# Performance work log

Hardware: AMD Instinct MI355X
Metric: run time of the kernel (lower is better)

The kernel has to match this reference:

```python
import jax, jax.numpy as jnp
import numpy as np

H = 64  # rnn_size == input_size

def setup_inputs() -> dict:
    key = jax.random.key(0)
    ks = jax.random.split(key, 6)
    vocab = 32000
    B, T = 4096, 128
    s = 1.0 / np.sqrt(H)
    return {
        "inst": jax.random.randint(ks[0], (B, T), 0, vocab, dtype=jnp.int64),
        "embed_w": jax.random.normal(ks[1], (vocab + 1, H), dtype=jnp.float32),
        "W_ih": jax.random.uniform(ks[2], (4 * H, H), dtype=jnp.float32, minval=-s, maxval=s),
        "W_hh": jax.random.uniform(ks[3], (4 * H, H), dtype=jnp.float32, minval=-s, maxval=s),
        "b_ih": jax.random.uniform(ks[4], (4 * H,), dtype=jnp.float32, minval=-s, maxval=s),
        "b_hh": jax.random.uniform(ks[5], (4 * H,), dtype=jnp.float32, minval=-s, maxval=s),
    }

def _lstm_scan(xs, W_ih, W_hh, b_ih, b_hh):
    # xs: [T, B, H]. PyTorch LSTMCell gate order: i, f, g, o.
    B = xs.shape[1]
    # Precompute input projections for all timesteps in one big GEMM.
    x_proj = jnp.einsum('tbh,gh->tbg', xs, W_ih) + b_ih + b_hh  # [T, B, 4H]

    def step(carry, xp):
        h, c = carry
        gates = xp + h @ W_hh.T  # [B, 4H]
        i, f, g, o = jnp.split(gates, 4, axis=-1)
        c = jax.nn.sigmoid(f) * c + jax.nn.sigmoid(i) * jnp.tanh(g)
        h = jax.nn.sigmoid(o) * jnp.tanh(c)
        return (h, c), None

    h0 = jnp.zeros((B, H), dtype=xs.dtype)
    c0 = jnp.zeros((B, H), dtype=xs.dtype)
    (h, c), _ = jax.lax.scan(step, (h0, c0), x_proj)
    return h

def reference(inst, embed_w, W_ih, W_hh, b_ih, b_hh):
    # inst: [B, T] int; embedding lookup for whole sequence at once.
    xs = embed_w[inst]                 # [B, T, H]
    xs = jnp.swapaxes(xs, 0, 1)        # [T, B, H] for scan over time
    return _lstm_scan(xs, W_ih, W_hh, b_ih, b_hh)  # final h: [B, H]
```

## Files before the change

### kernel.cpp

```cpp
#include <hip/hip_runtime.h>
#include <hip/hip_bf16.h>

#define H_DIM   64
#define T_STEPS 128
#define B_TOT   4096
#define BB      16
#define SK      72
#define NTHREADS 512

typedef _Float16 half8  __attribute__((ext_vector_type(8)));
typedef __fp16   fp16x2 __attribute__((ext_vector_type(2)));
typedef __attribute__((ext_vector_type(4))) float f32x4;

__device__ __forceinline__ float fast_sigmoid(float x) {
    float e = __expf(-x);
    return __builtin_amdgcn_rcpf(1.0f + e);
}
__device__ __forceinline__ float fast_tanh(float x) {
    float e2 = __expf(2.0f * x);
    return 1.0f - 2.0f * __builtin_amdgcn_rcpf(e2 + 1.0f);
}

__global__ __launch_bounds__(NTHREADS) void lstm_fused(
    const int* __restrict__ inst, const float* __restrict__ embed,
    const float* __restrict__ Wih, const float* __restrict__ Whh,
    const float* __restrict__ bih, const float* __restrict__ bhh,
    float* __restrict__ out)
{
    __shared__ __align__(16) _Float16 sX[2][BB][SK];
    __shared__ __align__(16) _Float16 sH[2][BB][SK];
    __shared__ int sInst[BB * T_STEPS];

    const int tid  = (int)threadIdx.x;
    const int w    = tid >> 6;
    const int l    = tid & 63;
    const int lrow = l & 15;
    const int lk   = l >> 4;
    const bool losd = (lrow < 8);
    const int c    = w * 8 + (lrow & 7);
    const int b0   = (int)blockIdx.x * BB;

    for (int i = tid; i < BB * T_STEPS; i += NTHREADS)
        sInst[i] = inst[b0 * T_STEPS + i];

    for (int i = tid; i < BB * SK; i += NTHREADS)
        ((_Float16*)sH)[i] = (_Float16)0.0f;
    __syncthreads();

    half8 wf[2][4];
    float bias[2];
#pragma unroll
    for (int q = 0; q < 2; ++q) {
        const int gate = q * 2 + (lrow >> 3);
        const int gcol = gate * 64 + c;
        bias[q] = bih[gcol] + bhh[gcol];
#pragma unroll
        for (int kf = 0; kf < 4; ++kf) {
            const float* src = (kf < 2 ? Wih : Whh) + (long)gcol * H_DIM + (kf & 1) * 32 + lk * 8;
            half8 v;
#pragma unroll
            for (int j = 0; j < 8; ++j) v[j] = (_Float16)src[j];
            wf[q][kf] = v;
        }
    }

    const int xr = tid >> 5;
    const int xc = tid & 31;
    {
        const int idx = sInst[xr * T_STEPS + 0];
        const float2 xv = *reinterpret_cast<const float2*>(embed + (long)idx * H_DIM + xc * 2);
        fp16x2 hp = __builtin_amdgcn_cvt_pkrtz(xv.x, xv.y);
        *reinterpret_cast<fp16x2*>(&sX[0][xr][xc * 2]) = hp;
    }
    __syncthreads();

    float creg[2] = {0.f, 0.f};
    float hreg[2] = {0.f, 0.f};

    for (int t = 0; t < T_STEPS; ++t) {
        const int buf = t & 1;
        const int ob  = buf ^ 1;
        const bool pf = (t + 1 < T_STEPS);

        float2 xv = {0.f, 0.f};
        if (pf) {
            const int idx = sInst[xr * T_STEPS + t + 1];
            xv = *reinterpret_cast<const float2*>(embed + (long)idx * H_DIM + xc * 2);
        }

        half8 a0 = *reinterpret_cast<const half8*>(&sX[buf][lrow][lk * 8]);
        half8 a1 = *reinterpret_cast<const half8*>(&sX[buf][lrow][32 + lk * 8]);
        half8 a2 = *reinterpret_cast<const half8*>(&sH[buf][lrow][lk * 8]);
        half8 a3 = *reinterpret_cast<const half8*>(&sH[buf][lrow][32 + lk * 8]);

        f32x4 acc[2];
#pragma unroll
        for (int q = 0; q < 2; ++q) {
            f32x4 pA = {bias[q], bias[q], bias[q], bias[q]};
            f32x4 pB = {0.f, 0.f, 0.f, 0.f};
            pA = __builtin_amdgcn_mfma_f32_16x16x32_f16(a0, wf[q][0], pA, 0, 0, 0);
            pB = __builtin_amdgcn_mfma_f32_16x16x32_f16(a1, wf[q][1], pB, 0, 0, 0);
            pA = __builtin_amdgcn_mfma_f32_16x16x32_f16(a2, wf[q][2], pA, 0, 0, 0);
            pB = __builtin_amdgcn_mfma_f32_16x16x32_f16(a3, wf[q][3], pB, 0, 0, 0);
            acc[q] = pA + pB;
        }

        const float e0 = __shfl_xor(losd ? acc[0][2] : acc[0][0], 8);
        const float e1 = __shfl_xor(losd ? acc[0][3] : acc[0][1], 8);
        const float e2 = __shfl_xor(losd ? acc[1][2] : acc[1][0], 8);
        const float e3 = __shfl_xor(losd ? acc[1][3] : acc[1][1], 8);

#pragma unroll
        for (int j = 0; j < 2; ++j) {
            const int r  = (losd ? 0 : 2) + j;
            const float ea = j ? e1 : e0;
            const float eb = j ? e3 : e2;
            const float vi = losd ? acc[0][r] : ea;
            const float vf = losd ? ea        : acc[0][r];
            const float vg = losd ? acc[1][r] : eb;
            const float vo = losd ? eb        : acc[1][r];
            const float iv = fast_sigmoid(vi);
            const float fv = fast_sigmoid(vf);
            const float gv = fast_tanh(vg);
            const float ov = fast_sigmoid(vo);
            const float cn = fv * creg[j] + iv * gv;
            creg[j] = cn;
            hreg[j] = ov * fast_tanh(cn);

            if (pf) {
                const int row = lk * 4 + r;
                sH[ob][row][c] = (_Float16)hreg[j];
            }
        }

        if (pf) {
            fp16x2 hp = __builtin_amdgcn_cvt_pkrtz(xv.x, xv.y);
            *reinterpret_cast<fp16x2*>(&sX[ob][xr][xc * 2]) = hp;
        }
        __syncthreads();
    }

#pragma unroll
    for (int j = 0; j < 2; ++j) {
        const int row = lk * 4 + (losd ? 0 : 2) + j;
        out[(long)(b0 + row) * H_DIM + c] = hreg[j];
    }
}

extern "C" void kernel_launch(void* const* d_in, const int* in_sizes, int n_in,
                              void* d_out, int out_size, void* d_ws, size_t ws_size,
                              hipStream_t stream) {
    const int*   inst  = (const int*)  d_in[0];
    const float* embed = (const float*)d_in[1];
    const float* Wih   = (const float*)d_in[2];
    const float* Whh   = (const float*)d_in[3];
    const float* bih   = (const float*)d_in[4];
    const float* bhh   = (const float*)d_in[5];
    float* out = (float*)d_out;

    lstm_fused<<<B_TOT / BB, NTHREADS, 0, stream>>>(inst, embed, Wih, Whh, bih, bhh, out);
}
```

Baseline: 90.87 us.

## Double threads per block, one gate-tile per wave, fold log2e into weights

Doubles the block to 16 waves so each wave computes one 16x16 MFMA gate tile (4 MFMAs per step instead of 8) and each lane produces a single h/c element, using a two-stage xor shuffle to gather the i,f,g,o gates. The log2(e) and 2·log2(e) scaling is folded into the fp16 weights and bias so activations use raw exp2 instead of exp plus a multiply. The embedding prefetch becomes one scalar-broadcast row per wave with one float per lane. The aim is to shorten the serial per-step critical path, in exchange for more barrier participants per step and extra shuffle and select work; scaling the weights before the fp16 conversion slightly changes rounding.

```diff
diff --git a/kernel.cpp b/kernel.cpp
--- a/kernel.cpp
+++ b/kernel.cpp
@@ -6,19 +6,23 @@
 #define B_TOT   4096
 #define BB      16
 #define SK      72
-#define NTHREADS 512
+#define NTHREADS 1024
 
 typedef _Float16 half8  __attribute__((ext_vector_type(8)));
 typedef __fp16   fp16x2 __attribute__((ext_vector_type(2)));
 typedef __attribute__((ext_vector_type(4))) float f32x4;
 
-__device__ __forceinline__ float fast_sigmoid(float x) {
-    float e = __expf(-x);
-    return __builtin_amdgcn_rcpf(1.0f + e);
+#if __has_builtin(__builtin_amdgcn_exp2f)
+#define EXP2(x) __builtin_amdgcn_exp2f(x)
+#else
+#define EXP2(x) exp2f(x)
+#endif
+
+__device__ __forceinline__ float sigmoid2(float xp) {
+    return __builtin_amdgcn_rcpf(1.0f + EXP2(-xp));
 }
-__device__ __forceinline__ float fast_tanh(float x) {
-    float e2 = __expf(2.0f * x);
-    return 1.0f - 2.0f * __builtin_amdgcn_rcpf(e2 + 1.0f);
+__device__ __forceinline__ float tanh2(float xp) {
+    return fmaf(-2.0f, __builtin_amdgcn_rcpf(EXP2(xp) + 1.0f), 1.0f);
 }
 
 __global__ __launch_bounds__(NTHREADS) void lstm_fused(
@@ -36,9 +40,14 @@
     const int l    = tid & 63;
     const int lrow = l & 15;
     const int lk   = l >> 4;
-    const bool losd = (lrow < 8);
-    const int c    = w * 8 + (lrow & 7);
+    const int g4   = lrow >> 2;
+    const bool g0  = g4 & 1;
+    const bool g1  = (g4 >> 1) & 1;
+    const int col  = w * 4 + (lrow & 3);
+    const int row  = lk * 4 + g4;
     const int b0   = (int)blockIdx.x * BB;
+
+    const float L2E = 1.4426950408889634f;
 
     for (int i = tid; i < BB * T_STEPS; i += NTHREADS)
         sInst[i] = inst[b0 * T_STEPS + i];
@@ -47,45 +56,39 @@
         ((_Float16*)sH)[i] = (_Float16)0.0f;
     __syncthreads();
 
-    half8 wf[2][4];
-    float bias[2];
-#pragma unroll
-    for (int q = 0; q < 2; ++q) {
-        const int gate = q * 2 + (lrow >> 3);
-        const int gcol = gate * 64 + c;
-        bias[q] = bih[gcol] + bhh[gcol];
+    const float wscale = (g4 == 2) ? 2.0f * L2E : L2E;
+    half8 wf[4];
+    float bias;
+    {
+        const int gcol = g4 * 64 + col;
+        bias = (bih[gcol] + bhh[gcol]) * wscale;
 #pragma unroll
         for (int kf = 0; kf < 4; ++kf) {
             const float* src = (kf < 2 ? Wih : Whh) + (long)gcol * H_DIM + (kf & 1) * 32 + lk * 8;
             half8 v;
 #pragma unroll
-            for (int j = 0; j < 8; ++j) v[j] = (_Float16)src[j];
-            wf[q][kf] = v;
+            for (int j = 0; j < 8; ++j) v[j] = (_Float16)(src[j] * wscale);
+            wf[kf] = v;
         }
     }
 
-    const int xr = tid >> 5;
-    const int xc = tid & 31;
     {
-        const int idx = sInst[xr * T_STEPS + 0];
-        const float2 xv = *reinterpret_cast<const float2*>(embed + (long)idx * H_DIM + xc * 2);
-        fp16x2 hp = __builtin_amdgcn_cvt_pkrtz(xv.x, xv.y);
-        *reinterpret_cast<fp16x2*>(&sX[0][xr][xc * 2]) = hp;
+        const int idx = __builtin_amdgcn_readfirstlane(sInst[w * T_STEPS + 0]);
+        sX[0][w][l] = (_Float16)embed[(long)idx * H_DIM + l];
     }
     __syncthreads();
 
-    float creg[2] = {0.f, 0.f};
-    float hreg[2] = {0.f, 0.f};
+    float creg = 0.f, hreg = 0.f;
 
     for (int t = 0; t < T_STEPS; ++t) {
         const int buf = t & 1;
         const int ob  = buf ^ 1;
         const bool pf = (t + 1 < T_STEPS);
 
-        float2 xv = {0.f, 0.f};
+        float xv = 0.f;
         if (pf) {
-            const int idx = sInst[xr * T_STEPS + t + 1];
-            xv = *reinterpret_cast<const float2*>(embed + (long)idx * H_DIM + xc * 2);
+            const int idx = __builtin_amdgcn_readfirstlane(sInst[w * T_STEPS + t + 1]);
+            xv = embed[(long)idx * H_DIM + l];
         }
 
         half8 a0 = *reinterpret_cast<const half8*>(&sX[buf][lrow][lk * 8]);
@@ -93,58 +96,47 @@
         half8 a2 = *reinterpret_cast<const half8*>(&sH[buf][lrow][lk * 8]);
         half8 a3 = *reinterpret_cast<const half8*>(&sH[buf][lrow][32 + lk * 8]);
 
-        f32x4 acc[2];
-#pragma unroll
-        for (int q = 0; q < 2; ++q) {
-            f32x4 pA = {bias[q], bias[q], bias[q], bias[q]};
-            f32x4 pB = {0.f, 0.f, 0.f, 0.f};
-            pA = __builtin_amdgcn_mfma_f32_16x16x32_f16(a0, wf[q][0], pA, 0, 0, 0);
-            pB = __builtin_amdgcn_mfma_f32_16x16x32_f16(a1, wf[q][1], pB, 0, 0, 0);
-            pA = __builtin_amdgcn_mfma_f32_16x16x32_f16(a2, wf[q][2], pA, 0, 0, 0);
-            pB = __builtin_amdgcn_mfma_f32_16x16x32_f16(a3, wf[q][3], pB, 0, 0, 0);
-            acc[q] = pA + pB;
-        }
+        f32x4 pA = {bias, bias, bias, bias};
+        f32x4 pB = {0.f, 0.f, 0.f, 0.f};
+        pA = __builtin_amdgcn_mfma_f32_16x16x32_f16(a0, wf[0], pA, 0, 0, 0);
+        pB = __builtin_amdgcn_mfma_f32_16x16x32_f16(a1, wf[1], pB, 0, 0, 0);
+        pA = __builtin_amdgcn_mfma_f32_16x16x32_f16(a2, wf[2], pA, 0, 0, 0);
+        pB = __builtin_amdgcn_mfma_f32_16x16x32_f16(a3, wf[3], pB, 0, 0, 0);
+        const f32x4 acc = pA + pB;
 
-        const float e0 = __shfl_xor(losd ? acc[0][2] : acc[0][0], 8);
-        const float e1 = __shfl_xor(losd ? acc[0][3] : acc[0][1], 8);
-        const float e2 = __shfl_xor(losd ? acc[1][2] : acc[1][0], 8);
-        const float e3 = __shfl_xor(losd ? acc[1][3] : acc[1][1], 8);
+        const float s1a = g0 ? acc[0] : acc[1];
+        const float s1b = g0 ? acc[2] : acc[3];
+        const float r1a = __shfl_xor(s1a, 4);
+        const float r1b = __shfl_xor(s1b, 4);
+        const float B0 = g0 ? r1a : acc[0];
+        const float B1 = g0 ? acc[1] : r1a;
+        const float B2 = g0 ? r1b : acc[2];
+        const float B3 = g0 ? acc[3] : r1b;
+        const float s2a = g1 ? B0 : B2;
+        const float s2b = g1 ? B1 : B3;
+        const float r2a = __shfl_xor(s2a, 8);
+        const float r2b = __shfl_xor(s2b, 8);
+        const float vi = g1 ? r2a : B0;
+        const float vf = g1 ? r2b : B1;
+        const float vg = g1 ? B2 : r2a;
+        const float vo = g1 ? B3 : r2b;
 
-#pragma unroll
-        for (int j = 0; j < 2; ++j) {
-            const int r  = (losd ? 0 : 2) + j;
-            const float ea = j ? e1 : e0;
-            const float eb = j ? e3 : e2;
-            const float vi = losd ? acc[0][r] : ea;
-            const float vf = losd ? ea        : acc[0][r];
-            const float vg = losd ? acc[1][r] : eb;
-            const float vo = losd ? eb        : acc[1][r];
-            const float iv = fast_sigmoid(vi);
-            const float fv = fast_sigmoid(vf);
-            const float gv = fast_tanh(vg);
-            const float ov = fast_sigmoid(vo);
-            const float cn = fv * creg[j] + iv * gv;
-            creg[j] = cn;
-            hreg[j] = ov * fast_tanh(cn);
-
-            if (pf) {
-                const int row = lk * 4 + r;
-                sH[ob][row][c] = (_Float16)hreg[j];
-            }
-        }
+        const float iv = sigmoid2(vi);
+        const float fv = sigmoid2(vf);
+        const float gv = tanh2(vg);
+        const float ov = sigmoid2(vo);
+        const float cn = fv * creg + iv * gv;
+        creg = cn;
+        hreg = ov * tanh2(cn * (2.0f * L2E));
 
         if (pf) {
-            fp16x2 hp = __builtin_amdgcn_cvt_pkrtz(xv.x, xv.y);
-            *reinterpret_cast<fp16x2*>(&sX[ob][xr][xc * 2]) = hp;
+            sH[ob][row][col] = (_Float16)hreg;
+            sX[ob][w][l] = (_Float16)xv;
         }
         __syncthreads();
     }
 
-#pragma unroll
-    for (int j = 0; j < 2; ++j) {
-        const int row = lk * 4 + (losd ? 0 : 2) + j;
-        out[(long)(b0 + row) * H_DIM + c] = hreg[j];
-    }
+    out[(long)(b0 + row) * H_DIM + col] = hreg;
 }
 
 extern "C" void kernel_launch(void* const* d_in, const int* in_sizes, int n_in,
```

Result: slower. 104.0 us (+14.4%).

## Batch embedding prefetch, fold log2e into weights, use DPP for lane swaps

Applied to the files above, without the earlier changes.

Embedding rows are now gathered eight timesteps at a time into a register buffer, so fewer global-load latencies sit inside each recurrent step. Weights and biases are pre-scaled by log2(e), or 2·log2(e) for the tanh gate, so the activations can call exp2 directly and skip a multiply. The xor-8 lane exchanges use DPP row_xmask instead of ds_bpermute shuffles. The cost is extra registers for the prefetch buffer and a slightly different fp16 rounding of the scaled weights.

```diff
diff --git a/kernel.cpp b/kernel.cpp
--- a/kernel.cpp
+++ b/kernel.cpp
@@ -7,18 +7,28 @@
 #define BB      16
 #define SK      72
 #define NTHREADS 512
+#define XBATCH  8
 
 typedef _Float16 half8  __attribute__((ext_vector_type(8)));
 typedef __fp16   fp16x2 __attribute__((ext_vector_type(2)));
 typedef __attribute__((ext_vector_type(4))) float f32x4;
 
-__device__ __forceinline__ float fast_sigmoid(float x) {
-    float e = __expf(-x);
-    return __builtin_amdgcn_rcpf(1.0f + e);
+#if __has_builtin(__builtin_amdgcn_exp2f)
+#define EXP2(x) __builtin_amdgcn_exp2f(x)
+#else
+#define EXP2(x) exp2f(x)
+#endif
+
+__device__ __forceinline__ float sigmoid2(float xp) {
+    return __builtin_amdgcn_rcpf(1.0f + EXP2(-xp));
 }
-__device__ __forceinline__ float fast_tanh(float x) {
-    float e2 = __expf(2.0f * x);
-    return 1.0f - 2.0f * __builtin_amdgcn_rcpf(e2 + 1.0f);
+__device__ __forceinline__ float tanh2(float xp) {
+    return fmaf(-2.0f, __builtin_amdgcn_rcpf(EXP2(xp) + 1.0f), 1.0f);
+}
+
+__device__ __forceinline__ float xor8_dpp(float v) {
+    return __int_as_float(__builtin_amdgcn_mov_dpp(
+        __float_as_int(v), 0x128 , 0xf, 0xf, false));
 }
 
 __global__ __launch_bounds__(NTHREADS) void lstm_fused(
@@ -40,6 +50,8 @@
     const int c    = w * 8 + (lrow & 7);
     const int b0   = (int)blockIdx.x * BB;
 
+    const float L2E = 1.4426950408889634f;
+
     for (int i = tid; i < BB * T_STEPS; i += NTHREADS)
         sInst[i] = inst[b0 * T_STEPS + i];
 
@@ -52,14 +64,15 @@
 #pragma unroll
     for (int q = 0; q < 2; ++q) {
         const int gate = q * 2 + (lrow >> 3);
+        const float wscale = (gate == 2) ? 2.0f * L2E : L2E;
         const int gcol = gate * 64 + c;
-        bias[q] = bih[gcol] + bhh[gcol];
+        bias[q] = (bih[gcol] + bhh[gcol]) * wscale;
 #pragma unroll
         for (int kf = 0; kf < 4; ++kf) {
             const float* src = (kf < 2 ? Wih : Whh) + (long)gcol * H_DIM + (kf & 1) * 32 + lk * 8;
             half8 v;
 #pragma unroll
-            for (int j = 0; j < 8; ++j) v[j] = (_Float16)src[j];
+            for (int j = 0; j < 8; ++j) v[j] = (_Float16)(src[j] * wscale);
             wf[q][kf] = v;
         }
     }
@@ -72,6 +85,13 @@
         fp16x2 hp = __builtin_amdgcn_cvt_pkrtz(xv.x, xv.y);
         *reinterpret_cast<fp16x2*>(&sX[0][xr][xc * 2]) = hp;
     }
+
+    float2 xbuf[XBATCH];
+#pragma unroll
+    for (int j = 0; j < XBATCH; ++j) {
+        const int idx = sInst[xr * T_STEPS + 1 + j];
+        xbuf[j] = *reinterpret_cast<const float2*>(embed + (long)idx * H_DIM + xc * 2);
+    }
     __syncthreads();
 
     float creg[2] = {0.f, 0.f};
@@ -82,10 +102,17 @@
         const int ob  = buf ^ 1;
         const bool pf = (t + 1 < T_STEPS);
 
-        float2 xv = {0.f, 0.f};
-        if (pf) {
-            const int idx = sInst[xr * T_STEPS + t + 1];
-            xv = *reinterpret_cast<const float2*>(embed + (long)idx * H_DIM + xc * 2);
+        const float2 xcur = xbuf[t & (XBATCH - 1)];
+
+        if ((t & (XBATCH - 1)) == (XBATCH - 1) && pf) {
+#pragma unroll
+            for (int j = 0; j < XBATCH; ++j) {
+                const int tt = t + 2 + j;
+                if (tt < T_STEPS) {
+                    const int idx = sInst[xr * T_STEPS + tt];
+                    xbuf[j] = *reinterpret_cast<const float2*>(embed + (long)idx * H_DIM + xc * 2);
+                }
+            }
         }
 
         half8 a0 = *reinterpret_cast<const half8*>(&sX[buf][lrow][lk * 8]);
@@ -105,10 +132,10 @@
             acc[q] = pA + pB;
         }
 
-        const float e0 = __shfl_xor(losd ? acc[0][2] : acc[0][0], 8);
-        const float e1 = __shfl_xor(losd ? acc[0][3] : acc[0][1], 8);
-        const float e2 = __shfl_xor(losd ? acc[1][2] : acc[1][0], 8);
-        const float e3 = __shfl_xor(losd ? acc[1][3] : acc[1][1], 8);
+        const float e0 = xor8_dpp(losd ? acc[0][2] : acc[0][0]);
+        const float e1 = xor8_dpp(losd ? acc[0][3] : acc[0][1]);
+        const float e2 = xor8_dpp(losd ? acc[1][2] : acc[1][0]);
+        const float e3 = xor8_dpp(losd ? acc[1][3] : acc[1][1]);
 
 #pragma unroll
         for (int j = 0; j < 2; ++j) {
@@ -119,13 +146,13 @@
             const float vf = losd ? ea        : acc[0][r];
             const float vg = losd ? acc[1][r] : eb;
             const float vo = losd ? eb        : acc[1][r];
-            const float iv = fast_sigmoid(vi);
-            const float fv = fast_sigmoid(vf);
-            const float gv = fast_tanh(vg);
-            const float ov = fast_sigmoid(vo);
+            const float iv = sigmoid2(vi);
+            const float fv = sigmoid2(vf);
+            const float gv = tanh2(vg);
+            const float ov = sigmoid2(vo);
             const float cn = fv * creg[j] + iv * gv;
             creg[j] = cn;
-            hreg[j] = ov * fast_tanh(cn);
+            hreg[j] = ov * tanh2(cn * (2.0f * L2E));
 
             if (pf) {
                 const int row = lk * 4 + r;
@@ -134,7 +161,7 @@
         }
 
         if (pf) {
-            fp16x2 hp = __builtin_amdgcn_cvt_pkrtz(xv.x, xv.y);
+            fp16x2 hp = __builtin_amdgcn_cvt_pkrtz(xcur.x, xcur.y);
             *reinterpret_cast<fp16x2*>(&sX[ob][xr][xc * 2]) = hp;
         }
         __syncthreads();
```

New measurement: 133.7 us. +47.2%, slower.
